# Performance work log

Hardware: AMD Instinct MI355X
Metric: run time of the kernel (lower is better)

Reference implementation:

```python
import jax, jax.numpy as jnp
import numpy as np

PC_START = (-51.2, -51.2)
VOXEL = (0.1, 0.1)
OUT_STRIDE = 4
NUM_POINT = 5


def setup_inputs() -> dict:
    key = jax.random.key(0)
    k1, k2, k3, k4, k5 = jax.random.split(key, 5)
    B, N, C, H, W = 4, 512, 256, 256, 256
    feats = jax.random.normal(k1, (B, C, H, W), dtype=jnp.float32)
    xy = jax.random.uniform(k2, (B, N, 2), minval=-45.0, maxval=45.0, dtype=jnp.float32)
    z = jax.random.uniform(k3, (B, N, 1), minval=-2.0, maxval=2.0, dtype=jnp.float32)
    dims = jax.random.uniform(k4, (B, N, 3), minval=1.0, maxval=5.0, dtype=jnp.float32)
    ry = jax.random.uniform(k5, (B, N, 1), minval=-np.pi, maxval=np.pi, dtype=jnp.float32)
    rois = jnp.concatenate([xy, z, dims, ry], axis=-1)  # [B,N,7]
    return {"spatial_features_2d": feats, "rois": rois}


def _corner_box2d(centers, dims, angles):
    # corners_nd order x0y0, x0y1, x1y1, x1y0 (torch [0,1,3,2] reorder), origin 0.5
    corners_norm = jnp.array([[0., 0.], [0., 1.], [1., 1.], [1., 0.]], dtype=centers.dtype) - 0.5
    corners = dims[:, None, :] * corners_norm[None]  # [N,4,2]
    c, s = jnp.cos(angles), jnp.sin(angles)
    # per-box rotation: out[n,i,k] = sum_j corners[n,i,j] * R[n,j,k], R = [[c,-s],[s,c]]
    R = jnp.stack([jnp.stack([c, -s], axis=-1), jnp.stack([s, c], axis=-1)], axis=-2)  # [N,2,2]
    corners = jnp.einsum('nij,njk->nik', corners, R)
    return corners + centers[:, None, :]


def _box_centers(box):
    # box: [N,7] -> points: [5N,3] (center, front, back, left, right midpoints)
    center2d = box[:, :2]
    height = box[:, 2:3]
    dim2d = box[:, 3:5]
    ry = box[:, -1]
    cor = _corner_box2d(center2d, dim2d, ry)  # [N,4,2]
    front = jnp.concatenate([(cor[:, 0] + cor[:, 1]) / 2, height], axis=-1)
    back = jnp.concatenate([(cor[:, 2] + cor[:, 3]) / 2, height], axis=-1)
    left = jnp.concatenate([(cor[:, 0] + cor[:, 3]) / 2, height], axis=-1)
    right = jnp.concatenate([(cor[:, 1] + cor[:, 2]) / 2, height], axis=-1)
    return jnp.concatenate([box[:, :3], front, back, left, right], axis=0)


def _bilinear(im, x, y):
    # im: [H,W,C]; x,y: [P]
    H, W, _ = im.shape
    xf = jnp.floor(x).astype(jnp.int32)
    yf = jnp.floor(y).astype(jnp.int32)
    x0 = jnp.clip(xf, 0, W - 1)
    x1 = jnp.clip(xf + 1, 0, W - 1)
    y0 = jnp.clip(yf, 0, H - 1)
    y1 = jnp.clip(yf + 1, 0, H - 1)
    Ia, Ib, Ic, Id = im[y0, x0], im[y1, x0], im[y0, x1], im[y1, x1]  # [P,C]
    x0f, x1f = x0.astype(x.dtype), x1.astype(x.dtype)
    y0f, y1f = y0.astype(y.dtype), y1.astype(y.dtype)
    wa = (x1f - x) * (y1f - y)
    wb = (x1f - x) * (y - y0f)
    wc = (x - x0f) * (y1f - y)
    wd = (x - x0f) * (y - y0f)
    return Ia * wa[:, None] + Ib * wb[:, None] + Ic * wc[:, None] + Id * wd[:, None]


def reference(spatial_features_2d, rois):
    # spatial_features_2d: [B,C,H,W]; rois: [B,N,7] -> roi_features: [B,N,NUM_POINT*C]
    bev = jnp.transpose(spatial_features_2d, (0, 2, 3, 1))  # [B,H,W,C]

    def per_batch(im, box):
        pts = _box_centers(box)  # [5N,3]
        xs = (pts[:, 0] - PC_START[0]) / VOXEL[0] / OUT_STRIDE
        ys = (pts[:, 1] - PC_START[1]) / VOXEL[1] / OUT_STRIDE
        fm = _bilinear(im, xs, ys)  # [5N,C]
        N = box.shape[0]
        # torch cat of NUM_POINT sections along channel dim == reshape/transpose
        return fm.reshape(NUM_POINT, N, -1).transpose(1, 0, 2).reshape(N, -1)

    return jax.vmap(per_batch)(bev, rois)
```

## Files before the change

kernel.cpp:

```cpp
#include <hip/hip_runtime.h>
#include <math.h>

constexpr int B = 4;
constexpr int N = 512;
constexpr int C = 256;
constexpr int H = 256;
constexpr int W = 256;
constexpr int NPT = 5;

__global__ __launch_bounds__(256)
void bev_extract_kernel(const float* __restrict__ feats,
                        const float* __restrict__ rois,
                        float* __restrict__ out)
{
    const int bn = blockIdx.x;
    const int b  = bn >> 9;
    const int c  = threadIdx.x;

    const float* roi = rois + (size_t)bn * 7;
    const float cx = roi[0];
    const float cy = roi[1];
    const float dx = roi[3];
    const float dy = roi[4];
    const float ry = roi[6];

    float si, co;
    sincosf(ry, &si, &co);
    const float hx = 0.5f * dx;
    const float hy = 0.5f * dy;

    float px[NPT], py[NPT];
    px[0] = cx;            py[0] = cy;
    px[1] = cx - hx * co;  py[1] = cy + hx * si;
    px[2] = cx + hx * co;  py[2] = cy - hx * si;
    px[3] = cx - hy * si;  py[3] = cy - hy * co;
    px[4] = cx + hy * si;  py[4] = cy + hy * co;

    const float* __restrict__ fp = feats + (((size_t)b * C + c) * H) * W;
    float* __restrict__ op = out + (size_t)bn * (NPT * C) + c;

#pragma unroll
    for (int p = 0; p < NPT; ++p) {
        const float xs = (px[p] + 51.2f) * 2.5f;
        const float ys = (py[p] + 51.2f) * 2.5f;
        const float xf = floorf(xs);
        const float yf = floorf(ys);
        int xi = (int)xf;
        int yi = (int)yf;
        const int x0 = min(max(xi, 0), W - 1);
        const int x1 = min(max(xi + 1, 0), W - 1);
        const int y0 = min(max(yi, 0), H - 1);
        const int y1 = min(max(yi + 1, 0), H - 1);

        const float x0f = (float)x0, x1f = (float)x1;
        const float y0f = (float)y0, y1f = (float)y1;
        const float wa = (x1f - xs) * (y1f - ys);
        const float wb = (x1f - xs) * (ys - y0f);
        const float wc = (xs - x0f) * (y1f - ys);
        const float wd = (xs - x0f) * (ys - y0f);

        const float Ia = fp[y0 * W + x0];
        const float Ib = fp[y1 * W + x0];
        const float Ic = fp[y0 * W + x1];
        const float Id = fp[y1 * W + x1];

        op[p * C] = Ia * wa + Ib * wb + Ic * wc + Id * wd;
    }
}

extern "C" void kernel_launch(void* const* d_in, const int* in_sizes, int n_in,
                              void* d_out, int out_size, void* d_ws, size_t ws_size,
                              hipStream_t stream) {
    const float* feats = (const float*)d_in[0];
    const float* rois  = (const float*)d_in[1];
    float* out = (float*)d_out;

    dim3 grid(B * N);
    dim3 block(C);
    bev_extract_kernel<<<grid, block, 0, stream>>>(feats, rois, out);
}
```

Before: 363.2 us.

## Restructure gather so each wave samples one channel plane across many points

```diff
diff --git a/kernel.cpp b/kernel.cpp
--- a/kernel.cpp
+++ b/kernel.cpp
@@ -7,46 +7,69 @@
 constexpr int H = 256;
 constexpr int W = 256;
 constexpr int NPT = 5;
+constexpr int PTS = N * NPT;
+constexpr int CHUNKS = 8;
+constexpr int PCHUNK = PTS / CHUNKS;
+constexpr int CG = 4;
+constexpr int NCG = C / CG;
+constexpr int NBLK = B * NCG * CHUNKS;
+
 
 __global__ __launch_bounds__(256)
-void bev_extract_kernel(const float* __restrict__ feats,
-                        const float* __restrict__ rois,
-                        float* __restrict__ out)
+void bev_gather_kernel(const float* __restrict__ feats,
+                       const float* __restrict__ rois,
+                       float* __restrict__ out)
 {
-    const int bn = blockIdx.x;
-    const int b  = bn >> 9;
-    const int c  = threadIdx.x;
+    const int i    = blockIdx.x;
+    const int xcd  = i & 7;
+    const int k    = i >> 3;
+    const int grp  = xcd * 32 + (k & 31);
+    const int chunk= k >> 5;
+    const int b    = grp >> 6;
+    const int cg   = grp & 63;
 
-    const float* roi = rois + (size_t)bn * 7;
-    const float cx = roi[0];
-    const float cy = roi[1];
-    const float dx = roi[3];
-    const float dy = roi[4];
-    const float ry = roi[6];
+    const int tid  = threadIdx.x;
+    const int wave = tid >> 6;
+    const int lane = tid & 63;
+    const int c    = cg * CG + wave;
 
-    float si, co;
-    sincosf(ry, &si, &co);
-    const float hx = 0.5f * dx;
-    const float hy = 0.5f * dy;
+    __shared__ float sxs[PCHUNK];
+    __shared__ float sys[PCHUNK];
+    __shared__ float svals[PCHUNK][CG + 1];
 
-    float px[NPT], py[NPT];
-    px[0] = cx;            py[0] = cy;
-    px[1] = cx - hx * co;  py[1] = cy + hx * si;
-    px[2] = cx + hx * co;  py[2] = cy - hx * si;
-    px[3] = cx - hy * si;  py[3] = cy - hy * co;
-    px[4] = cx + hy * si;  py[4] = cy + hy * co;
+    const int qbase = chunk * PCHUNK;
 
-    const float* __restrict__ fp = feats + (((size_t)b * C + c) * H) * W;
-    float* __restrict__ op = out + (size_t)bn * (NPT * C) + c;
+    for (int q = tid; q < PCHUNK; q += 256) {
+        const int qq = qbase + q;
+        const int n  = qq / NPT;
+        const int p  = qq - n * NPT;
+        const float* roi = rois + ((size_t)b * N + n) * 7;
+        const float cx = roi[0], cy = roi[1];
+        const float hx = 0.5f * roi[3];
+        const float hy = 0.5f * roi[4];
+        float si, co;
+        sincosf(roi[6], &si, &co);
+        float px = cx, py = cy;
+        if      (p == 1) { px = cx - hx * co; py = cy + hx * si; }
+        else if (p == 2) { px = cx + hx * co; py = cy - hx * si; }
+        else if (p == 3) { px = cx - hy * si; py = cy - hy * co; }
+        else if (p == 4) { px = cx + hy * si; py = cy + hy * co; }
+        sxs[q] = (px + 51.2f) * 2.5f;
+        sys[q] = (py + 51.2f) * 2.5f;
+    }
+    __syncthreads();
+
+    const float* __restrict__ fp = feats + ((size_t)b * C + c) * (H * W);
 
 #pragma unroll
-    for (int p = 0; p < NPT; ++p) {
-        const float xs = (px[p] + 51.2f) * 2.5f;
-        const float ys = (py[p] + 51.2f) * 2.5f;
+    for (int j = 0; j < PCHUNK / 64; ++j) {
+        const int q = j * 64 + lane;
+        const float xs = sxs[q];
+        const float ys = sys[q];
         const float xf = floorf(xs);
         const float yf = floorf(ys);
-        int xi = (int)xf;
-        int yi = (int)yf;
+        const int xi = (int)xf;
+        const int yi = (int)yf;
         const int x0 = min(max(xi, 0), W - 1);
         const int x1 = min(max(xi + 1, 0), W - 1);
         const int y0 = min(max(yi, 0), H - 1);
@@ -64,7 +87,17 @@
         const float Ic = fp[y0 * W + x1];
         const float Id = fp[y1 * W + x1];
 
-        op[p * C] = Ia * wa + Ib * wb + Ic * wc + Id * wd;
+        svals[q][wave] = Ia * wa + Ib * wb + Ic * wc + Id * wd;
+    }
+    __syncthreads();
+
+    for (int q = tid; q < PCHUNK; q += 256) {
+        const int qq = qbase + q;
+        const int n  = qq / NPT;
+        const int p  = qq - n * NPT;
+        float4 v = make_float4(svals[q][0], svals[q][1], svals[q][2], svals[q][3]);
+        float* op = out + (((size_t)(b * N + n) * NPT + p) * C + cg * CG);
+        *reinterpret_cast<float4*>(op) = v;
     }
 }
 
@@ -75,7 +108,5 @@
     const float* rois  = (const float*)d_in[1];
     float* out = (float*)d_out;
 
-    dim3 grid(B * N);
-    dim3 block(C);
-    bev_extract_kernel<<<grid, block, 0, stream>>>(feats, rois, out);
+    bev_gather_kernel<<<dim3(NBLK), dim3(256), 0, stream>>>(feats, rois, out);
 }
```

New measurement: 367.8 us. No clear change (+1.3%).
